# Kernel tuning notes

Hardware: AMD Instinct MI355X
Metric: run time of the kernel (lower is better)

Reference implementation:

```python
import jax, jax.numpy as jnp
import numpy as np

D_IN, D_HID, D_OUT = 256, 512, 256
N_EXPERTS, TOP_K = 64, 2
B, S = 8, 4096


def setup_inputs() -> dict:
    key = jax.random.key(0)
    ks = jax.random.split(key, 8)
    scale_in = 1.0 / np.sqrt(D_IN)
    scale_hid = 1.0 / np.sqrt(D_HID)
    return {
        "x": jax.random.normal(ks[0], (B, S, D_IN), dtype=jnp.float32),
        "Wr": jax.random.uniform(ks[1], (D_IN, N_EXPERTS), jnp.float32, -scale_in, scale_in),
        "br": jax.random.uniform(ks[2], (N_EXPERTS,), jnp.float32, -scale_in, scale_in),
        "W1": jax.random.uniform(ks[3], (N_EXPERTS, D_IN, D_HID), jnp.float32, -scale_in, scale_in),
        "b1": jax.random.uniform(ks[4], (N_EXPERTS, D_HID), jnp.float32, -scale_in, scale_in),
        "W2": jax.random.uniform(ks[5], (N_EXPERTS, D_HID, D_OUT), jnp.float32, -scale_hid, scale_hid),
        "b2": jax.random.uniform(ks[6], (N_EXPERTS, D_OUT), jnp.float32, -scale_hid, scale_hid),
    }


def reference(x, Wr, br, W1, b1, W2, b2):
    Bx, Sx, D = x.shape
    xf = x.reshape(-1, D)                                  # [T, D]
    T = xf.shape[0]
    E = Wr.shape[1]
    logits = xf @ Wr + br                                  # [T, E]
    topk_logits, topk_idx = jax.lax.top_k(logits, TOP_K)   # [T, K]
    gates = jax.nn.softmax(topk_logits, axis=1)            # softmax over selected k
    # dense combine weights: zero except at selected experts
    combine = jnp.zeros((T, E), xf.dtype).at[
        jnp.arange(T)[:, None], topk_idx].add(gates)       # [T, E]
    out = jnp.zeros((T, W2.shape[-1]), xf.dtype)
    for e in range(E):  # fixed small expert loop; each token weighted by combine mask
        h = jax.nn.relu(xf @ W1[e] + b1[e])                # [T, D_HID]
        y = h @ W2[e] + b2[e]                              # [T, D_OUT]
        out = out + combine[:, e:e + 1] * y
    return out.reshape(Bx, Sx, -1)
```

## Files before the change

### kernel.cpp

```cpp
#include <hip/hip_runtime.h>
#include <stdint.h>

#define T_TOK 32768
#define DIN   256
#define DHID  512
#define DOUT  256
#define NEXP  64
#define L1_SLOTS 4
#define L2_SLOTS 4
#define ROUTER_BLOCKS (T_TOK / 64)
#define PREP_BLOCKS   8192
#define XBF_BLOCKS    1024
#define L1_BLOCKS (NEXP * 4 * L1_SLOTS)
#define L2_BLOCKS (NEXP * 2 * L2_SLOTS)
#define CMB_BLOCKS (T_TOK / 8)

typedef __attribute__((ext_vector_type(8))) short short8;
typedef __attribute__((ext_vector_type(4))) float f32x4;

#define OFF_W1F   0u
#define OFF_W2F   16777216u
#define OFF_BASE  33554432u
#define OFF_CNT   (OFF_BASE + 0u)
#define OFF_CUR   (OFF_BASE + 256u)
#define OFF_OFFS  (OFF_BASE + 512u)
#define OFF_TOPKE (OFF_BASE + 2048u)
#define OFF_TOPKG (OFF_TOPKE + 262144u)
#define OFF_PERM  (OFF_TOPKG + 262144u)
#define OFF_PGATE (OFF_PERM + 262144u)
#define OFF_ISLOT (OFF_PGATE + 262144u)
#define OFF_XBF   (OFF_BASE + 2097152u)
#define OFF_H     (OFF_XBF + 16777216u)
#define OFF_YP    (OFF_H + 67108864u)

__device__ __forceinline__ unsigned short f2bf(float f) {
    union { float f; unsigned u; } a; a.f = f;
    unsigned u = a.u;
    u += 0x7fffu + ((u >> 16) & 1u);
    return (unsigned short)(u >> 16);
}
__device__ __forceinline__ unsigned pack2(float a, float b) {
    return (unsigned)f2bf(a) | ((unsigned)f2bf(b) << 16);
}
__device__ __forceinline__ float bf2f(unsigned short u) {
    union { unsigned u; float f; } a; a.u = (unsigned)u << 16; return a.f;
}

__device__ __forceinline__ void async_copy16(const uint4* g, uint4* l) {
    __builtin_amdgcn_global_load_lds(
        (const __attribute__((address_space(1))) unsigned int*)g,
        (__attribute__((address_space(3))) unsigned int*)l, 16, 0, 0);
}

__global__ __launch_bounds__(256) void router_prep(const float* __restrict__ x,
                                                   const float* __restrict__ Wr,
                                                   const float* __restrict__ br,
                                                   const float* __restrict__ W1,
                                                   const float* __restrict__ W2,
                                                   uint4* __restrict__ W1f,
                                                   uint4* __restrict__ W2f,
                                                   int* __restrict__ topk_e,
                                                   float* __restrict__ topk_g,
                                                   int* __restrict__ cnt,
                                                   unsigned* __restrict__ xbf) {
    __shared__ float xl[64][68];
    __shared__ float wt[64][68];
    __shared__ int lcnt[NEXP];
    int tid = threadIdx.x;

    if (blockIdx.x >= ROUTER_BLOCKS + PREP_BLOCKS) {
        int blk = blockIdx.x - (ROUTER_BLOCKS + PREP_BLOCKS);
        const float2* xs = (const float2*)x;
#pragma unroll
        for (int k = 0; k < 16; ++k) {
            int o = blk * 4096 + k * 256 + tid;
            float2 v = xs[o];
            xbf[o] = pack2(v.x, v.y);
        }
        return;
    }
    if (blockIdx.x >= ROUTER_BLOCKS) {
        int g = (blockIdx.x - ROUTER_BLOCKS) * 256 + tid;
        int isW2 = g >> 20;
        int gg = g & ((1 << 20) - 1);
        int l = gg & 63;
        int t = gg >> 6;
        int e = t >> 8;
        int rem = t & 255;
        int quad = l >> 4, lr = l & 15;
        float v[8];
        if (!isW2) {
            int nt = rem >> 3, kt = rem & 7;
            int kb = kt * 32 + quad * 8;
            int n = nt * 16 + lr;
            const float* s = W1 + (size_t)e * DIN * DHID + n;
#pragma unroll
            for (int j = 0; j < 8; ++j) v[j] = s[(size_t)(kb + j) * DHID];
        } else {
            int nt = rem >> 4, kt = rem & 15;
            int kb = kt * 32 + quad * 8;
            int n = nt * 16 + lr;
            const float* s = W2 + (size_t)e * DHID * DOUT + n;
#pragma unroll
            for (int j = 0; j < 8; ++j) v[j] = s[(size_t)(kb + j) * DOUT];
        }
        uint4 o;
        o.x = pack2(v[0], v[1]); o.y = pack2(v[2], v[3]);
        o.z = pack2(v[4], v[5]); o.w = pack2(v[6], v[7]);
        (isW2 ? W2f : W1f)[gg] = o;
        return;
    }

    if (tid < NEXP) lcnt[tid] = 0;
    int a = tid >> 4;
    int bcol = tid & 15;
    int tok0 = blockIdx.x * 64;
    float c[4][4];
#pragma unroll
    for (int i = 0; i < 4; ++i)
#pragma unroll
        for (int j = 0; j < 4; ++j) c[i][j] = 0.0f;

    for (int chunk = 0; chunk < 4; ++chunk) {
        int d0 = chunk * 64;
        {
            int tok = tid >> 2, off = (tid & 3) * 16;
            const float4* s = (const float4*)(x + (size_t)(tok0 + tok) * DIN + d0 + off);
            float4* d = (float4*)&xl[tok][off];
#pragma unroll
            for (int i = 0; i < 4; ++i) d[i] = s[i];
        }
        {
            int dd = tid >> 2, ecol = (tid & 3) * 16;
            const float* s = Wr + (size_t)(d0 + dd) * NEXP + ecol;
#pragma unroll
            for (int j = 0; j < 16; ++j) wt[ecol + j][dd] = s[j];
        }
        __syncthreads();
#pragma unroll 4
        for (int d = 0; d < 64; d += 4) {
            float4 xv[4], wv[4];
#pragma unroll
            for (int i = 0; i < 4; ++i) xv[i] = *(const float4*)&xl[bcol + i * 16][d];
#pragma unroll
            for (int j = 0; j < 4; ++j) wv[j] = *(const float4*)&wt[a + j * 16][d];
#pragma unroll
            for (int i = 0; i < 4; ++i)
#pragma unroll
                for (int j = 0; j < 4; ++j) {
                    c[i][j] = fmaf(xv[i].x, wv[j].x, c[i][j]);
                    c[i][j] = fmaf(xv[i].y, wv[j].y, c[i][j]);
                    c[i][j] = fmaf(xv[i].z, wv[j].z, c[i][j]);
                    c[i][j] = fmaf(xv[i].w, wv[j].w, c[i][j]);
                }
        }
        __syncthreads();
    }
#pragma unroll
    for (int i = 0; i < 4; ++i)
#pragma unroll
        for (int j = 0; j < 4; ++j)
            xl[bcol + i * 16][a + j * 16] = c[i][j] + br[a + j * 16];
    __syncthreads();

    int w = tid >> 6, lane = tid & 63;
    for (int ti = 0; ti < 16; ++ti) {
        int tl = w * 16 + ti;
        float acc = xl[tl][lane];
        float v = acc; int idx = lane;
#pragma unroll
        for (int m = 32; m; m >>= 1) {
            float ov = __shfl_xor(v, m); int oi = __shfl_xor(idx, m);
            if (ov > v || (ov == v && oi < idx)) { v = ov; idx = oi; }
        }
        int e0 = idx; float l0 = v;
        float v2 = (lane == e0) ? -3.4e38f : acc; int idx2 = lane;
#pragma unroll
        for (int m = 32; m; m >>= 1) {
            float ov = __shfl_xor(v2, m); int oi = __shfl_xor(idx2, m);
            if (ov > v2 || (ov == v2 && oi < idx2)) { v2 = ov; idx2 = oi; }
        }
        if (lane == 0) {
            int t = tok0 + tl;
            float ex = expf(v2 - l0);
            float g1 = ex / (1.0f + ex);
            topk_e[2 * t] = e0; topk_e[2 * t + 1] = idx2;
            topk_g[2 * t] = 1.0f - g1; topk_g[2 * t + 1] = g1;
            atomicAdd(&lcnt[e0], 1);
            atomicAdd(&lcnt[idx2], 1);
        }
    }
    __syncthreads();
    if (tid < NEXP) atomicAdd(&cnt[tid], lcnt[tid]);
}

__global__ __launch_bounds__(256) void scatter_kernel(const int* __restrict__ topk_e,
                                                      const float* __restrict__ topk_g,
                                                      const int* __restrict__ cnt,
                                                      int* __restrict__ cursor,
                                                      int* __restrict__ perm,
                                                      int* __restrict__ islot,
                                                      int* __restrict__ offs_g) {
    __shared__ int lcnt[NEXP], lbase[NEXP], sOffs[NEXP];
    int tid = threadIdx.x;
    if (tid < NEXP) lcnt[tid] = 0;
    if (tid < 64) {
        int c = cnt[tid];
        int ic = c;
#pragma unroll
        for (int d = 1; d < 64; d <<= 1) {
            int vc = __shfl_up(ic, d);
            if (tid >= d) ic += vc;
        }
        sOffs[tid] = ic - c;
        if (blockIdx.x == 0) {
            offs_g[tid] = ic - c;
            if (tid == 63) offs_g[64] = ic;
        }
    }
    __syncthreads();
    int t = blockIdx.x * 256 + tid;
    int e0 = topk_e[2 * t], e1 = topk_e[2 * t + 1];
    int i0 = atomicAdd(&lcnt[e0], 1);
    int i1 = atomicAdd(&lcnt[e1], 1);
    __syncthreads();
    if (tid < NEXP) lbase[tid] = atomicAdd(&cursor[tid], lcnt[tid]);
    __syncthreads();
    int p0 = sOffs[e0] + lbase[e0] + i0;
    int p1 = sOffs[e1] + lbase[e1] + i1;
    perm[p0] = t;
    perm[p1] = t;
    islot[2 * t] = p0;
    islot[2 * t + 1] = p1;
}

__global__ __launch_bounds__(512, 4) void expert_l1(const unsigned short* __restrict__ xbf,
                                                    const uint4* __restrict__ W1f,
                                                    const float* __restrict__ b1,
                                                    const int* __restrict__ cnt,
                                                    const int* __restrict__ offs,
                                                    const int* __restrict__ perm,
                                                    unsigned short* __restrict__ H) {
    __shared__ uint4 Wlds[4096];
    __shared__ int toks[256];
    __shared__ float b1s[128];

    int tid = threadIdx.x, bx = blockIdx.x;
    int ns = bx & 3, slot = (bx >> 2) & 3, e = bx >> 4;
    int ne = cnt[e];
    if (slot * 256 >= ne) return;
    int base = offs[e];
    int w = tid >> 6, lane = tid & 63, quad = lane >> 4, lr = lane & 15;

    const uint4* src = W1f + (size_t)(e * 256 + ns * 64) * 64;
#pragma unroll
    for (int r = 0; r < 8; ++r)
        async_copy16(src + r * 512 + w * 64 + lane, Wlds + r * 512 + w * 64);
    if (tid < 32)
        *(float4*)&b1s[tid * 4] =
            *(const float4*)(b1 + (size_t)e * DHID + ns * 128 + tid * 4);

    for (int mc = slot; mc * 256 < ne; mc += L1_SLOTS) {
        __syncthreads();
        if (tid < 256) {
            int idx = mc * 256 + tid;
            toks[tid] = perm[base + (idx < ne ? idx : ne - 1)];
        }
        __syncthreads();

        short8 a[2][8];
#pragma unroll
        for (int mt = 0; mt < 2; ++mt) {
            const unsigned short* xr =
                xbf + (size_t)toks[(w * 2 + mt) * 16 + lr] * DIN + quad * 8;
#pragma unroll
            for (int kt = 0; kt < 8; ++kt) a[mt][kt] = *(const short8*)(xr + kt * 32);
        }

#pragma unroll
        for (int ntb = 0; ntb < 4; ++ntb) {
            f32x4 acc[2][2];
#pragma unroll
            for (int i = 0; i < 2; ++i)
#pragma unroll
                for (int m = 0; m < 2; ++m) acc[i][m] = (f32x4){0.f, 0.f, 0.f, 0.f};
#pragma unroll
            for (int kt = 0; kt < 8; ++kt) {
                short8 B0 = *(const short8*)&Wlds[((ntb * 2 + 0) * 8 + kt) * 64 + lane];
                short8 B1 = *(const short8*)&Wlds[((ntb * 2 + 1) * 8 + kt) * 64 + lane];
#pragma unroll
                for (int mt = 0; mt < 2; ++mt) {
                    acc[0][mt] = __builtin_amdgcn_mfma_f32_16x16x32_bf16(a[mt][kt], B0, acc[0][mt], 0, 0, 0);
                    acc[1][mt] = __builtin_amdgcn_mfma_f32_16x16x32_bf16(a[mt][kt], B1, acc[1][mt], 0, 0, 0);
                }
            }
#pragma unroll
            for (int nt2 = 0; nt2 < 2; ++nt2) {
                int nloc = ntb * 32 + nt2 * 16 + lr;
                float bias = b1s[nloc];
#pragma unroll
                for (int mt = 0; mt < 2; ++mt)
#pragma unroll
                    for (int r = 0; r < 4; ++r) {
                        int idx = mc * 256 + (w * 2 + mt) * 16 + quad * 4 + r;
                        if (idx < ne)
                            H[(size_t)(base + idx) * DHID + ns * 128 + nloc] =
                                f2bf(fmaxf(acc[nt2][mt][r] + bias, 0.0f));
                    }
            }
        }
    }
}

__global__ __launch_bounds__(512, 4) void expert_l2(const unsigned short* __restrict__ H,
                                                    const uint4* __restrict__ W2f,
                                                    const float* __restrict__ b2,
                                                    const int* __restrict__ cnt,
                                                    const int* __restrict__ offs,
                                                    unsigned short* __restrict__ yp) {
    __shared__ uint4 Wlds[4096];
    __shared__ float b2s[128];

    int tid = threadIdx.x, bx = blockIdx.x;
    int ns = bx & 1, slot = (bx >> 1) & 3, e = bx >> 3;
    int ne = cnt[e];
    if (slot * 256 >= ne) return;
    int base = offs[e];
    int w = tid >> 6, lane = tid & 63, quad = lane >> 4, lr = lane & 15;

    if (tid < 32)
        *(float4*)&b2s[tid * 4] =
            *(const float4*)(b2 + (size_t)e * DOUT + ns * 128 + tid * 4);

    for (int mc = slot; mc * 256 < ne; mc += L2_SLOTS) {
        int row0 = mc * 256 + (w * 2 + 0) * 16 + lr;
        int row1 = mc * 256 + (w * 2 + 1) * 16 + lr;
        if (row0 >= ne) row0 = ne - 1;
        if (row1 >= ne) row1 = ne - 1;
        const unsigned short* h0 = H + (size_t)(base + row0) * DHID + quad * 8;
        const unsigned short* h1 = H + (size_t)(base + row1) * DHID + quad * 8;

        f32x4 acc[8][2];
#pragma unroll
        for (int nt = 0; nt < 8; ++nt)
#pragma unroll
            for (int mt = 0; mt < 2; ++mt) acc[nt][mt] = (f32x4){0.f, 0.f, 0.f, 0.f};

#pragma unroll
        for (int kh = 0; kh < 2; ++kh) {
            __syncthreads();
#pragma unroll
            for (int nt = 0; nt < 8; ++nt) {
                const uint4* src = W2f + (size_t)(e * 256 + (ns * 8 + nt) * 16 + kh * 8) * 64;
                async_copy16(src + w * 64 + lane, Wlds + nt * 512 + w * 64);
            }
            __syncthreads();

            short8 a[8][2];
#pragma unroll
            for (int kt = 0; kt < 8; ++kt) {
                a[kt][0] = *(const short8*)(h0 + kh * 256 + kt * 32);
                a[kt][1] = *(const short8*)(h1 + kh * 256 + kt * 32);
            }
#pragma unroll
            for (int kt = 0; kt < 8; ++kt) {
#pragma unroll
                for (int nt = 0; nt < 8; ++nt) {
                    short8 B = *(const short8*)&Wlds[(nt * 8 + kt) * 64 + lane];
                    acc[nt][0] = __builtin_amdgcn_mfma_f32_16x16x32_bf16(a[kt][0], B, acc[nt][0], 0, 0, 0);
                    acc[nt][1] = __builtin_amdgcn_mfma_f32_16x16x32_bf16(a[kt][1], B, acc[nt][1], 0, 0, 0);
                }
            }
        }

#pragma unroll
        for (int nt = 0; nt < 8; ++nt) {
            int nloc = nt * 16 + lr;
            float bias = b2s[nloc];
#pragma unroll
            for (int mt = 0; mt < 2; ++mt)
#pragma unroll
                for (int r = 0; r < 4; ++r) {
                    int crow = mc * 256 + (w * 2 + mt) * 16 + quad * 4 + r;
                    if (crow < ne)
                        yp[(size_t)(base + crow) * DOUT + ns * 128 + nloc] =
                            f2bf(acc[nt][mt][r] + bias);
                }
        }
    }
}

__global__ __launch_bounds__(256) void combine_out(const unsigned short* __restrict__ yp,
                                                   const int* __restrict__ islot,
                                                   const float* __restrict__ topk_g,
                                                   float* __restrict__ out) {
    int tid = threadIdx.x;
    int tok = blockIdx.x * 8 + (tid >> 5);
    int cseg = (tid & 31) * 8;
    int p0 = islot[2 * tok], p1 = islot[2 * tok + 1];
    float g0 = topk_g[2 * tok], g1 = topk_g[2 * tok + 1];
    short8 v0 = *(const short8*)(yp + (size_t)p0 * DOUT + cseg);
    short8 v1 = *(const short8*)(yp + (size_t)p1 * DOUT + cseg);
    float4 o0, o1;
    o0.x = g0 * bf2f((unsigned short)v0[0]) + g1 * bf2f((unsigned short)v1[0]);
    o0.y = g0 * bf2f((unsigned short)v0[1]) + g1 * bf2f((unsigned short)v1[1]);
    o0.z = g0 * bf2f((unsigned short)v0[2]) + g1 * bf2f((unsigned short)v1[2]);
    o0.w = g0 * bf2f((unsigned short)v0[3]) + g1 * bf2f((unsigned short)v1[3]);
    o1.x = g0 * bf2f((unsigned short)v0[4]) + g1 * bf2f((unsigned short)v1[4]);
    o1.y = g0 * bf2f((unsigned short)v0[5]) + g1 * bf2f((unsigned short)v1[5]);
    o1.z = g0 * bf2f((unsigned short)v0[6]) + g1 * bf2f((unsigned short)v1[6]);
    o1.w = g0 * bf2f((unsigned short)v0[7]) + g1 * bf2f((unsigned short)v1[7]);
    float* d = out + (size_t)tok * DOUT + cseg;
    *(float4*)d = o0;
    *(float4*)(d + 4) = o1;
}

extern "C" void kernel_launch(void* const* d_in, const int* in_sizes, int n_in,
                              void* d_out, int out_size, void* d_ws, size_t ws_size,
                              hipStream_t stream) {
    (void)in_sizes; (void)n_in; (void)ws_size; (void)out_size;
    const float* x  = (const float*)d_in[0];
    const float* Wr = (const float*)d_in[1];
    const float* br = (const float*)d_in[2];
    const float* W1 = (const float*)d_in[3];
    const float* b1 = (const float*)d_in[4];
    const float* W2 = (const float*)d_in[5];
    const float* b2 = (const float*)d_in[6];
    float* out = (float*)d_out;
    char* ws = (char*)d_ws;

    uint4*    W1f    = (uint4*)(ws + OFF_W1F);
    uint4*    W2f    = (uint4*)(ws + OFF_W2F);
    int*      cnt    = (int*)(ws + OFF_CNT);
    int*      cursor = (int*)(ws + OFF_CUR);
    int*      offs   = (int*)(ws + OFF_OFFS);
    int*      topk_e = (int*)(ws + OFF_TOPKE);
    float*    topk_g = (float*)(ws + OFF_TOPKG);
    int*      perm   = (int*)(ws + OFF_PERM);
    int*      islot  = (int*)(ws + OFF_ISLOT);
    unsigned* xbf    = (unsigned*)(ws + OFF_XBF);
    unsigned short* Hbuf = (unsigned short*)(ws + OFF_H);
    unsigned short* ypb  = (unsigned short*)(ws + OFF_YP);

    hipMemsetAsync(ws + OFF_CNT, 0, 512, stream);

    router_prep<<<ROUTER_BLOCKS + PREP_BLOCKS + XBF_BLOCKS, 256, 0, stream>>>(
        x, Wr, br, W1, W2, W1f, W2f, topk_e, topk_g, cnt, xbf);
    scatter_kernel<<<T_TOK / 256, 256, 0, stream>>>(topk_e, topk_g, cnt, cursor,
                                                    perm, islot, offs);
    expert_l1<<<L1_BLOCKS, 512, 0, stream>>>((const unsigned short*)xbf, W1f, b1,
                                             cnt, offs, perm, Hbuf);
    expert_l2<<<L2_BLOCKS, 512, 0, stream>>>(Hbuf, W2f, b2, cnt, offs, ypb);
    combine_out<<<CMB_BLOCKS, 256, 0, stream>>>(ypb, islot, topk_g, out);
}
```

Measured before the change: 301.8 us.

## Double-buffer W2 LDS tiles in expert_l2 to overlap loads with MFMA

Splits the expert_l2 K loop into four phases with two LDS buffers. Each phase issues async copies of the next W2 slice before running the MFMAs on the current one, and one barrier per phase replaces two. Each wave now loads the K tiles of a single output tile, and launch bounds drop from 4 to 2 blocks per CU, which allows more registers per thread. The aim is to hide global-to-LDS latency behind compute, in exchange for more register pressure and a lower occupancy cap.

```diff
diff --git a/kernel.cpp b/kernel.cpp
--- a/kernel.cpp
+++ b/kernel.cpp
@@ -312,13 +312,13 @@
     }
 }
 
-__global__ __launch_bounds__(512, 4) void expert_l2(const unsigned short* __restrict__ H,
+__global__ __launch_bounds__(512, 2) void expert_l2(const unsigned short* __restrict__ H,
                                                     const uint4* __restrict__ W2f,
                                                     const float* __restrict__ b2,
                                                     const int* __restrict__ cnt,
                                                     const int* __restrict__ offs,
                                                     unsigned short* __restrict__ yp) {
-    __shared__ uint4 Wlds[4096];
+    __shared__ uint4 Wlds[2][2048];
     __shared__ float b2s[128];
 
     int tid = threadIdx.x, bx = blockIdx.x;
@@ -331,6 +331,8 @@
     if (tid < 32)
         *(float4*)&b2s[tid * 4] =
             *(const float4*)(b2 + (size_t)e * DOUT + ns * 128 + tid * 4);
+
+    const uint4* wsrc = W2f + (size_t)(e * 256 + (ns * 8 + w) * 16) * 64;
 
     for (int mc = slot; mc * 256 < ne; mc += L2_SLOTS) {
         int row0 = mc * 256 + (w * 2 + 0) * 16 + lr;
@@ -347,30 +349,32 @@
             for (int mt = 0; mt < 2; ++mt) acc[nt][mt] = (f32x4){0.f, 0.f, 0.f, 0.f};
 
 #pragma unroll
-        for (int kh = 0; kh < 2; ++kh) {
+        for (int i = 0; i < 4; ++i)
+            async_copy16(wsrc + i * 64 + lane, &Wlds[0][w * 256 + i * 64]);
+
+#pragma unroll
+        for (int p = 0; p < 4; ++p) {
             __syncthreads();
-#pragma unroll
-            for (int nt = 0; nt < 8; ++nt) {
-                const uint4* src = W2f + (size_t)(e * 256 + (ns * 8 + nt) * 16 + kh * 8) * 64;
-                async_copy16(src + w * 64 + lane, Wlds + nt * 512 + w * 64);
+            short8 a0[4], a1[4];
+#pragma unroll
+            for (int ktl = 0; ktl < 4; ++ktl) {
+                a0[ktl] = *(const short8*)(h0 + (p * 4 + ktl) * 32);
+                a1[ktl] = *(const short8*)(h1 + (p * 4 + ktl) * 32);
             }
-            __syncthreads();
-
-            short8 a[8][2];
-#pragma unroll
-            for (int kt = 0; kt < 8; ++kt) {
-                a[kt][0] = *(const short8*)(h0 + kh * 256 + kt * 32);
-                a[kt][1] = *(const short8*)(h1 + kh * 256 + kt * 32);
+            if (p < 3) {
+#pragma unroll
+                for (int i = 0; i < 4; ++i)
+                    async_copy16(wsrc + (size_t)((p + 1) * 4 + i) * 64 + lane,
+                                 &Wlds[(p + 1) & 1][w * 256 + i * 64]);
             }
 #pragma unroll
-            for (int kt = 0; kt < 8; ++kt) {
+            for (int ktl = 0; ktl < 4; ++ktl)
 #pragma unroll
                 for (int nt = 0; nt < 8; ++nt) {
-                    short8 B = *(const short8*)&Wlds[(nt * 8 + kt) * 64 + lane];
-                    acc[nt][0] = __builtin_amdgcn_mfma_f32_16x16x32_bf16(a[kt][0], B, acc[nt][0], 0, 0, 0);
-                    acc[nt][1] = __builtin_amdgcn_mfma_f32_16x16x32_bf16(a[kt][1], B, acc[nt][1], 0, 0, 0);
+                    short8 B = *(const short8*)&Wlds[p & 1][(nt * 4 + ktl) * 64 + lane];
+                    acc[nt][0] = __builtin_amdgcn_mfma_f32_16x16x32_bf16(a0[ktl], B, acc[nt][0], 0, 0, 0);
+                    acc[nt][1] = __builtin_amdgcn_mfma_f32_16x16x32_bf16(a1[ktl], B, acc[nt][1], 0, 0, 0);
                 }
-            }
         }
 
 #pragma unroll
```

Result: faster. 291.9 us (-3.3%).
